# Performance work log

Hardware: AMD Instinct MI355X
Metric: run time of the kernel (lower is better)

## Reference

```python
import jax, jax.numpy as jnp
import numpy as np

T_, N_, DIN, D, HEADS, WW, E_, DPE = 8, 20000, 128, 128, 4, 4, 320000, 8
DH = D // HEADS
NEG = -1e30
EPS_GATE = 1e-6


def setup_inputs() -> dict:
    key = jax.random.key(0)
    ks = jax.random.split(key, 10)
    return {
        "H_tilde": jax.random.normal(ks[0], (T_, N_, DIN), jnp.float32),
        "S": jax.random.uniform(ks[1], (T_, N_), jnp.float32),
        "Wq": jax.random.normal(ks[2], (D, DIN), jnp.float32) * 0.05,
        "Wkh": jax.random.normal(ks[3], (D, DIN), jnp.float32) * 0.05,
        "Wkpe": jax.random.normal(ks[4], (D, DPE), jnp.float32) * 0.05,
        "Wv": jax.random.normal(ks[5], (D, DIN), jnp.float32) * 0.05,
        "pe_table": jax.random.normal(ks[6], (WW + 1, DPE), jnp.float32),
        "rel_bias": jax.random.normal(ks[7], (WW + 1,), jnp.float32),
        "src": jax.random.randint(ks[8], (E_,), 0, N_),
        "dst": jax.random.randint(ks[9], (E_,), 0, N_),
    }


def reference(H_tilde, S, Wq, Wkh, Wkpe, Wv, pe_table, rel_bias, src, dst):
    T, N, _ = H_tilde.shape
    H, dh, W = HEADS, DH, WW
    scale = dh ** -0.5
    dtype = H_tilde.dtype

    # Projections (torch Linear: x @ W.T). W_k over concat([H, pe]) splits additively.
    Q = (H_tilde @ Wq.T).reshape(T, N, H, dh)
    K0 = (H_tilde @ Wkh.T).reshape(T, N, H, dh)
    V = (H_tilde @ Wv.T).reshape(T, N, H, dh)
    pe_k = (pe_table @ Wkpe.T).reshape(W + 1, H, dh)
    gate = jnp.log(jnp.clip(S, 0.0, 1.0) + EPS_GATE)  # (T, N)

    # Pad W zero-steps in front so a length-(W+1) slice at t covers t-W..t.
    pad = lambda x: jnp.concatenate([jnp.zeros((W,) + x.shape[1:], x.dtype), x], axis=0)
    Kp, Vp, gp = pad(K0), pad(V), pad(gate)

    def step(_, tq):
        t, Qt = tq  # Qt: (N, H, dh)
        Kwin = jax.lax.dynamic_slice_in_dim(Kp, t, W + 1, 0)[::-1]  # (W+1,N,H,dh), dt=0..W
        Vwin = jax.lax.dynamic_slice_in_dim(Vp, t, W + 1, 0)[::-1]
        gwin = jax.lax.dynamic_slice_in_dim(gp, t, W + 1, 0)[::-1]  # (W+1, N)
        Qd = Qt[dst]  # (E, H, dh)

        scores = []
        for dt in range(W + 1):
            Ks = Kwin[dt][src] + pe_k[dt][None]  # (E, H, dh)
            s = (jnp.einsum('ehc,ehc->eh', Qd, Ks) * scale
                 + rel_bias[dt] + gwin[dt][src][:, None])
            scores.append(jnp.where(dt <= t, s, NEG))  # mask dt > t (W_eff = min(W, t))
        sc = jnp.stack(scores)  # (W+1, E, H)

        # Segment softmax over incoming edges of each dst node, jointly over dt.
        mx = jax.ops.segment_max(sc.transpose(1, 0, 2), dst, num_segments=N)  # (N,W+1,H)
        mx = mx.max(axis=1)  # (N, H)
        valid = (jnp.arange(W + 1) <= t)[:, None, None]
        ex = jnp.where(valid, jnp.exp(sc - mx[dst][None]), 0.0)  # (W+1, E, H)

        denom = jax.ops.segment_sum(ex.sum(axis=0), dst, num_segments=N)  # (N, H)
        numer = jnp.zeros((N, H, dh), dtype)
        for dt in range(W + 1):
            contrib = ex[dt][:, :, None] * Vwin[dt][src]  # (E, H, dh)
            numer = numer + jax.ops.segment_sum(contrib, dst, num_segments=N)

        msg = numer / jnp.maximum(denom, 1e-12)[:, :, None]  # (N, H, dh)
        return None, msg.reshape(N, H * dh)

    _, M_out = jax.lax.scan(step, None, (jnp.arange(T), Q))
    return M_out  # (T, N, d)
```

## Files before the change

### kernel.cpp

```cpp
#include <hip/hip_runtime.h>

typedef unsigned short u16;
typedef unsigned int u32;
typedef __attribute__((ext_vector_type(8))) __bf16 bf16x8;
typedef __attribute__((ext_vector_type(4))) float f32x4;
typedef __attribute__((ext_vector_type(4))) _Float16 f16x4;
typedef __attribute__((ext_vector_type(2))) unsigned u32x2;

constexpr int TT = 8, NN = 20000, DD = 128, EE = 320000;
constexpr int MAXDEG = 64;
constexpr float SCL = 0.17677669529663687f;
constexpr int VBLK2 = 544;

__device__ __forceinline__ u16 f2bf(float f) {
  return __builtin_bit_cast(u16, (__bf16)f);
}
__device__ __forceinline__ u16 f2h(float f) {
  return __builtin_bit_cast(u16, (_Float16)f);
}
__device__ __forceinline__ float blo(u32 u) { return __uint_as_float(u << 16); }
__device__ __forceinline__ float bhi(u32 u) { return __uint_as_float(u & 0xffff0000u); }

__device__ __forceinline__ bf16x8 cvt8(float4 f0, float4 f1) {
  bf16x8 r;
  r[0] = (__bf16)f0.x; r[1] = (__bf16)f0.y; r[2] = (__bf16)f0.z; r[3] = (__bf16)f0.w;
  r[4] = (__bf16)f1.x; r[5] = (__bf16)f1.y; r[6] = (__bf16)f1.z; r[7] = (__bf16)f1.w;
  return r;
}

__global__ void k_init(const float* __restrict__ pe_table, const float* __restrict__ Wkpe,
                       const float* __restrict__ Wq, const float* __restrict__ Wkh,
                       const float* __restrict__ Wv,
                       float* __restrict__ pek, int* __restrict__ cnt,
                       u16* __restrict__ Wb) {
  int i = blockIdx.x * 256 + threadIdx.x;
  if (i < NN) cnt[i] = 0;
  if (i < 5 * DD) {
    int dt = i >> 7, j = i & 127;
    float s = 0.f;
    for (int p = 0; p < 8; ++p) s += pe_table[dt * 8 + p] * Wkpe[j * 8 + p];
    pek[i] = s;
  }
  if (i < 3 * DD * DD) {
    int y = i / (DD * DD), idx = i % (DD * DD);
    const float* W = (y == 0) ? Wq : (y == 1) ? Wkh : Wv;
    Wb[i] = f2bf(W[idx]);
  }
}

__global__ void k_build(const int* __restrict__ src, const int* __restrict__ dst,
                        int* __restrict__ cnt, int* __restrict__ eslot) {
  int i = blockIdx.x * 256 + threadIdx.x;
  if (i < EE) {
    int d = dst[i];
    int p = atomicAdd(&cnt[d], 1);
    if (p < MAXDEG) eslot[d * MAXDEG + p] = src[i];
  }
}

__global__ __launch_bounds__(256) void k_proj5(
    const float* __restrict__ Hm, const u16* __restrict__ Wb,
    u16* __restrict__ Qb, u16* __restrict__ Kb, u16* __restrict__ Vb) {
  int tid = threadIdx.x;
  int lane = tid & 63, wv = tid >> 6;
  int wr = wv >> 1, wc = wv & 1;
  int l15 = lane & 15, lq = lane >> 4;
  size_t m0 = (size_t)blockIdx.x * 128;

  for (int y = 0; y < 3; ++y) {
    u16* Out = (y == 0) ? Qb : (y == 1) ? Kb : Vb;
    const bool asF16 = (y == 2);
    const u16* Wy = Wb + y * DD * DD;

    f32x4 acc[4][4];
    for (int i = 0; i < 4; ++i)
      for (int j = 0; j < 4; ++j) acc[i][j] = (f32x4){0.f, 0.f, 0.f, 0.f};

    for (int ks = 0; ks < 4; ++ks) {
      int col0 = ks * 32 + lq * 8;
      bf16x8 a[4], b[4];
#pragma unroll
      for (int i = 0; i < 4; ++i) {
        const float* gp = Hm + (m0 + wr * 64 + i * 16 + l15) * DD + col0;
        a[i] = cvt8(*(const float4*)gp, *(const float4*)(gp + 4));
      }
#pragma unroll
      for (int j = 0; j < 4; ++j)
        b[j] = *(const bf16x8*)(Wy + (wc * 64 + j * 16 + l15) * DD + col0);
#pragma unroll
      for (int i = 0; i < 4; ++i)
#pragma unroll
        for (int j = 0; j < 4; ++j)
          acc[i][j] = __builtin_amdgcn_mfma_f32_16x16x32_bf16(a[i], b[j], acc[i][j], 0, 0, 0);
    }

#pragma unroll
    for (int i = 0; i < 4; ++i)
#pragma unroll
      for (int j = 0; j < 4; ++j)
#pragma unroll
        for (int g = 0; g < 4; ++g) {
          size_t row = m0 + wr * 64 + i * 16 + lq * 4 + g;
          int col = wc * 64 + j * 16 + l15;
          Out[row * DD + col] = asF16 ? f2h(acc[i][j][g]) : f2bf(acc[i][j][g]);
        }
  }
}

__global__ __launch_bounds__(256) void k_etab(const u16* __restrict__ Qb,
                                              const float* __restrict__ pek,
                                              const float* __restrict__ relb,
                                              float* __restrict__ Etab) {
  int t = blockIdx.y;
  int n = blockIdx.x * 64 + (threadIdx.x >> 2);
  int h = threadIdx.x & 3;
  if (n >= NN) return;
  const u16* qp = Qb + ((size_t)t * NN + n) * DD + h * 32;
  float q[32];
#pragma unroll
  for (int u = 0; u < 4; ++u) {
    uint4 qv = *(const uint4*)(qp + u * 8);
    q[u*8+0]=blo(qv.x); q[u*8+1]=bhi(qv.x); q[u*8+2]=blo(qv.y); q[u*8+3]=bhi(qv.y);
    q[u*8+4]=blo(qv.z); q[u*8+5]=bhi(qv.z); q[u*8+6]=blo(qv.w); q[u*8+7]=bhi(qv.w);
  }
#pragma unroll
  for (int d = 0; d < 5; ++d) {
    float s = 0.f;
#pragma unroll
    for (int c = 0; c < 32; ++c) s += q[c] * pek[d * DD + h * 32 + c];
    Etab[((size_t)(t * 5 + d) * NN + n) * 4 + h] = __expf(s * SCL + relb[d]);
  }
}

__global__ __launch_bounds__(256, 8) void k_agg8(
    const u16* __restrict__ Qb, const u16* __restrict__ Kb, const u16* __restrict__ Vb,
    const float* __restrict__ Sarr, const float* __restrict__ Etab,
    const int* __restrict__ cnt, const int* __restrict__ eslot,
    float* __restrict__ outp) {
  __shared__ int srcS[MAXDEG];
  __shared__ float eS[40][4];
  __shared__ u16 VldsS[4][VBLK2];
  int tid = threadIdx.x;
  const int h = tid >> 6, lane = tid & 63;
  const int n = blockIdx.x;

  int deg = min(cnt[n], MAXDEG);
  if (tid < MAXDEG) srcS[tid] = (tid < deg) ? eslot[n * MAXDEG + tid] : 0;
  if (tid < 160) {
    int p = tid >> 2, hh = tid & 3;
    eS[p][hh] = Etab[((size_t)p * NN + n) * 4 + hh];
  }
  __syncthreads();

  const int t16 = lane & 15, qo = lane >> 4, qo4 = qo * 4;
  const int h32 = h * 32;

  uint4 qb;
  {
    bool qok = t16 < 8;
    const u16* Qp = Qb + ((size_t)(t16 & 7) * NN + n) * DD + h32 + qo * 8;
    qb = qok ? *(const uint4*)(Qp) : make_uint4(0u, 0u, 0u, 0u);
  }

  f32x4 num0 = (f32x4){0.f, 0.f, 0.f, 0.f};
  f32x4 num1 = (f32x4){0.f, 0.f, 0.f, 0.f};
  float dd = 0.f;

  if (deg > 0) {
    const int degm1 = deg - 1;
    const int nch = (deg + 15) >> 4;
    const int cmax = nch << 4;
    const int nj = nch * 8;

    const int vkey = lane >> 2, vcb = lane & 3;
    u16* vbuf = &VldsS[h][0];
    unsigned trbase = (unsigned)(uintptr_t)vbuf + lane * 8;
    unsigned woff = (unsigned)((vcb >> 1) * VBLK2 + (vkey >> 2) * 128 +
                               (vkey & 3) * 32 + (vcb & 1) * 16);

    auto loadK = [&](int tp, int c16) -> uint4 {
      return *(const uint4*)(Kb + (size_t)tp * (NN * DD)
                             + (size_t)srcS[min(c16 + t16, degm1)] * DD + h32 + qo * 8);
    };
    auto loadV = [&](int tp, int c16) -> uint4 {
      return *(const uint4*)(Vb + (size_t)tp * (NN * DD)
                             + (size_t)srcS[min(c16 + vkey, degm1)] * DD + h32 + vcb * 8);
    };
    auto loadSg = [&](int tp, int c16) -> float {
      float s = Sarr[(size_t)tp * NN + srcS[min(c16 + t16, degm1)]];
      return fminf(fmaxf(s, 0.f), 1.f) + 1e-6f;
    };
    auto writeV = [&](uint4 f) { *(uint4*)((char*)vbuf + woff) = f; };
    auto compute = [&](uint4 ka, float sg, int tp, int c16) {
      int dt = t16 - tp;
      bool tval = (dt >= 0) && (dt <= 4) && (t16 < 8);
      float Ef = tval ? eS[t16 * 5 + dt][h] : 0.f;

      f32x4 z = (f32x4){0.f, 0.f, 0.f, 0.f};
      f32x4 sc = __builtin_amdgcn_mfma_f32_16x16x32_bf16(
          __builtin_bit_cast(bf16x8, ka), __builtin_bit_cast(bf16x8, qb), z, 0, 0, 0);

      f16x4 wf;
      float w0, w1, w2, w3;
      {
        float g0 = __shfl(sg, qo4 + 0), g1 = __shfl(sg, qo4 + 1);
        float g2 = __shfl(sg, qo4 + 2), g3 = __shfl(sg, qo4 + 3);
        g0 = ((c16 + qo4 + 0) < deg) ? g0 : 0.f;
        g1 = ((c16 + qo4 + 1) < deg) ? g1 : 0.f;
        g2 = ((c16 + qo4 + 2) < deg) ? g2 : 0.f;
        g3 = ((c16 + qo4 + 3) < deg) ? g3 : 0.f;
        w0 = __expf(sc[0] * SCL) * Ef * g0;
        w1 = __expf(sc[1] * SCL) * Ef * g1;
        w2 = __expf(sc[2] * SCL) * Ef * g2;
        w3 = __expf(sc[3] * SCL) * Ef * g3;
      }
      dd += w0 + w1 + w2 + w3;
      wf[0] = (_Float16)w0; wf[1] = (_Float16)w1;
      wf[2] = (_Float16)w2; wf[3] = (_Float16)w3;

      __builtin_amdgcn_sched_barrier(0);
      u32x2 vr0, vr1;
      asm volatile("ds_read_b64_tr_b16 %0, %1" : "=v"(vr0) : "v"(trbase));
      asm volatile("ds_read_b64_tr_b16 %0, %1 offset:544" : "=v"(vr1) : "v"(trbase));
      asm volatile("s_waitcnt lgkmcnt(0)");
      __builtin_amdgcn_sched_barrier(0);
      num0 = __builtin_amdgcn_mfma_f32_16x16x16f16(
          wf, __builtin_bit_cast(f16x4, vr0), num0, 0, 0, 0);
      num1 = __builtin_amdgcn_mfma_f32_16x16x16f16(
          wf, __builtin_bit_cast(f16x4, vr1), num1, 0, 0, 0);
    };

    uint4 kA = loadK(0, 0);
    float sgA = loadSg(0, 0);
    writeV(loadV(0, 0));
    int tpj = 0, cj = 0;
    int tpn = 0, cn = 16;
    if (cn >= cmax) { cn = 0; tpn = 1; }

    for (int j = 0; j < nj; ++j) {
      bool more = (j + 1) < nj;
      uint4 kB = make_uint4(0u, 0u, 0u, 0u), vB = make_uint4(0u, 0u, 0u, 0u);
      float sgB = 0.f;
      if (more) {
        kB = loadK(tpn, cn);
        vB = loadV(tpn, cn);
        sgB = loadSg(tpn, cn);
      }
      compute(kA, sgA, tpj, cj);
      __builtin_amdgcn_sched_barrier(0);
      if (more) writeV(vB);
      kA = kB;
      sgA = sgB;
      tpj = tpn; cj = cn;
      cn += 16;
      if (cn >= cmax) { cn = 0; ++tpn; }
    }
  }

  float Dh = dd;
  Dh += __shfl_xor(Dh, 16);
  Dh += __shfl_xor(Dh, 32);
#pragma unroll
  for (int r = 0; r < 4; ++r) {
    int t = qo4 + r;
    float Dt = __shfl(Dh, t);
    if (t < 8) {
      float inv = 1.f / fmaxf(Dt, 1e-12f);
      float* op = outp + ((size_t)t * NN + n) * DD + h32;
      op[t16] = num0[r] * inv;
      op[16 + t16] = num1[r] * inv;
    }
  }
}

extern "C" void kernel_launch(void* const* d_in, const int* in_sizes, int n_in,
                              void* d_out, int out_size, void* d_ws, size_t ws_size,
                              hipStream_t stream) {
  const float* Hm = (const float*)d_in[0];
  const float* S = (const float*)d_in[1];
  const float* Wq = (const float*)d_in[2];
  const float* Wkh = (const float*)d_in[3];
  const float* Wkpe = (const float*)d_in[4];
  const float* Wv = (const float*)d_in[5];
  const float* pe_table = (const float*)d_in[6];
  const float* relb = (const float*)d_in[7];
  const int* src = (const int*)d_in[8];
  const int* dst = (const int*)d_in[9];
  float* out = (float*)d_out;

  auto aup = [](size_t x) { return (x + 255) & ~(size_t)255; };
  char* base = (char*)d_ws;
  size_t off = 0;
  u16* Qb = (u16*)(base + off); off = aup(off + (size_t)TT * NN * DD * 2);
  u16* Kb = (u16*)(base + off); off = aup(off + (size_t)TT * NN * DD * 2);
  u16* Vb = (u16*)(base + off); off = aup(off + (size_t)TT * NN * DD * 2);
  float* pek = (float*)(base + off); off = aup(off + (size_t)5 * DD * 4);
  float* Etab = (float*)(base + off); off = aup(off + (size_t)TT * 5 * NN * 4 * 4);
  int* cnt = (int*)(base + off); off = aup(off + (size_t)NN * 4);
  int* eslot = (int*)(base + off); off = aup(off + (size_t)NN * MAXDEG * 4);
  u16* Wb = (u16*)(base + off); off = aup(off + (size_t)3 * DD * DD * 2);
  (void)ws_size; (void)in_sizes; (void)n_in; (void)out_size;

  k_init<<<(3 * DD * DD + 255) / 256, 256, 0, stream>>>(pe_table, Wkpe, Wq, Wkh, Wv,
                                                        pek, cnt, Wb);
  k_build<<<(EE + 255) / 256, 256, 0, stream>>>(src, dst, cnt, eslot);
  k_proj5<<<1250, 256, 0, stream>>>(Hm, Wb, Qb, Kb, Vb);
  k_etab<<<dim3((NN + 63) / 64, TT), 256, 0, stream>>>(Qb, pek, relb, Etab);
  k_agg8<<<NN, 256, 0, stream>>>(Qb, Kb, Vb, S, Etab, cnt, eslot, out);
}
```

Measured before the change: 365.2 us.

## Fuse edge-bias table into aggregation and reorder loop edge-chunk-outer, time-inner

Removes the separate k_etab kernel and its Etab buffer. The aggregation kernel now computes the per-node Q·pe_k plus rel_bias logits itself, using lane shuffles, and stores them in LDS. The clamped gate S is precomputed once in k_init into SgT. The main loop changes to edge-chunk outer and time-step inner, so each neighbour index and its offsets are fetched once and reused across all 8 timesteps, and the bias is folded into the exp argument. This saves one kernel launch and a global table round-trip, and moves the gate values to LDS per step. In exchange each block does a little more prologue work and adds LDS writes and reads per step.

```diff
diff --git a/kernel.cpp b/kernel.cpp
--- a/kernel.cpp
+++ b/kernel.cpp
@@ -30,9 +30,9 @@
 
 __global__ void k_init(const float* __restrict__ pe_table, const float* __restrict__ Wkpe,
                        const float* __restrict__ Wq, const float* __restrict__ Wkh,
-                       const float* __restrict__ Wv,
+                       const float* __restrict__ Wv, const float* __restrict__ S,
                        float* __restrict__ pek, int* __restrict__ cnt,
-                       u16* __restrict__ Wb) {
+                       u16* __restrict__ Wb, float* __restrict__ SgT) {
   int i = blockIdx.x * 256 + threadIdx.x;
   if (i < NN) cnt[i] = 0;
   if (i < 5 * DD) {
@@ -45,6 +45,9 @@
     int y = i / (DD * DD), idx = i % (DD * DD);
     const float* W = (y == 0) ? Wq : (y == 1) ? Wkh : Wv;
     Wb[i] = f2bf(W[idx]);
+  }
+  if (i < TT * NN) {
+    SgT[i] = fminf(fmaxf(S[i], 0.f), 1.f) + 1e-6f;
   }
 }
 
@@ -107,38 +110,15 @@
   }
 }
 
-__global__ __launch_bounds__(256) void k_etab(const u16* __restrict__ Qb,
-                                              const float* __restrict__ pek,
-                                              const float* __restrict__ relb,
-                                              float* __restrict__ Etab) {
-  int t = blockIdx.y;
-  int n = blockIdx.x * 64 + (threadIdx.x >> 2);
-  int h = threadIdx.x & 3;
-  if (n >= NN) return;
-  const u16* qp = Qb + ((size_t)t * NN + n) * DD + h * 32;
-  float q[32];
-#pragma unroll
-  for (int u = 0; u < 4; ++u) {
-    uint4 qv = *(const uint4*)(qp + u * 8);
-    q[u*8+0]=blo(qv.x); q[u*8+1]=bhi(qv.x); q[u*8+2]=blo(qv.y); q[u*8+3]=bhi(qv.y);
-    q[u*8+4]=blo(qv.z); q[u*8+5]=bhi(qv.z); q[u*8+6]=blo(qv.w); q[u*8+7]=bhi(qv.w);
-  }
-#pragma unroll
-  for (int d = 0; d < 5; ++d) {
-    float s = 0.f;
-#pragma unroll
-    for (int c = 0; c < 32; ++c) s += q[c] * pek[d * DD + h * 32 + c];
-    Etab[((size_t)(t * 5 + d) * NN + n) * 4 + h] = __expf(s * SCL + relb[d]);
-  }
-}
-
-__global__ __launch_bounds__(256, 8) void k_agg8(
+__global__ __launch_bounds__(256, 8) void k_agg9(
     const u16* __restrict__ Qb, const u16* __restrict__ Kb, const u16* __restrict__ Vb,
-    const float* __restrict__ Sarr, const float* __restrict__ Etab,
+    const float* __restrict__ SgT, const float* __restrict__ pek,
+    const float* __restrict__ relb,
     const int* __restrict__ cnt, const int* __restrict__ eslot,
     float* __restrict__ outp) {
   __shared__ int srcS[MAXDEG];
-  __shared__ float eS[40][4];
+  __shared__ float eL[4][40];
+  __shared__ float sgS[4][16];
   __shared__ u16 VldsS[4][VBLK2];
   int tid = threadIdx.x;
   const int h = tid >> 6, lane = tid & 63;
@@ -146,14 +126,10 @@
 
   int deg = min(cnt[n], MAXDEG);
   if (tid < MAXDEG) srcS[tid] = (tid < deg) ? eslot[n * MAXDEG + tid] : 0;
-  if (tid < 160) {
-    int p = tid >> 2, hh = tid & 3;
-    eS[p][hh] = Etab[((size_t)p * NN + n) * 4 + hh];
-  }
-  __syncthreads();
 
   const int t16 = lane & 15, qo = lane >> 4, qo4 = qo * 4;
   const int h32 = h * 32;
+  const int e6 = t16 * 6;
 
   uint4 qb;
   {
@@ -162,98 +138,98 @@
     qb = qok ? *(const uint4*)(Qp) : make_uint4(0u, 0u, 0u, 0u);
   }
 
+  {
+    float qf0 = blo(qb.x), qf1 = bhi(qb.x), qf2 = blo(qb.y), qf3 = bhi(qb.y);
+    float qf4 = blo(qb.z), qf5 = bhi(qb.z), qf6 = blo(qb.w), qf7 = bhi(qb.w);
+#pragma unroll
+    for (int d = 0; d < 5; ++d) {
+      const float* pp = pek + d * DD + h32 + qo * 8;
+      float4 p0 = *(const float4*)pp;
+      float4 p1 = *(const float4*)(pp + 4);
+      float s = qf0 * p0.x + qf1 * p0.y + qf2 * p0.z + qf3 * p0.w
+              + qf4 * p1.x + qf5 * p1.y + qf6 * p1.z + qf7 * p1.w;
+      s += __shfl_xor(s, 16);
+      s += __shfl_xor(s, 32);
+      if (qo == 0 && t16 < 8) eL[h][t16 * 5 + d] = s * SCL + relb[d];
+    }
+  }
+  __syncthreads();
+
   f32x4 num0 = (f32x4){0.f, 0.f, 0.f, 0.f};
   f32x4 num1 = (f32x4){0.f, 0.f, 0.f, 0.f};
   float dd = 0.f;
 
   if (deg > 0) {
     const int degm1 = deg - 1;
-    const int nch = (deg + 15) >> 4;
-    const int cmax = nch << 4;
-    const int nj = nch * 8;
-
-    const int vkey = lane >> 2, vcb = lane & 3;
     u16* vbuf = &VldsS[h][0];
     unsigned trbase = (unsigned)(uintptr_t)vbuf + lane * 8;
+    const int vkey = lane >> 2, vcb = lane & 3;
     unsigned woff = (unsigned)((vcb >> 1) * VBLK2 + (vkey >> 2) * 128 +
                                (vkey & 3) * 32 + (vcb & 1) * 16);
 
-    auto loadK = [&](int tp, int c16) -> uint4 {
-      return *(const uint4*)(Kb + (size_t)tp * (NN * DD)
-                             + (size_t)srcS[min(c16 + t16, degm1)] * DD + h32 + qo * 8);
-    };
-    auto loadV = [&](int tp, int c16) -> uint4 {
-      return *(const uint4*)(Vb + (size_t)tp * (NN * DD)
-                             + (size_t)srcS[min(c16 + vkey, degm1)] * DD + h32 + vcb * 8);
-    };
-    auto loadSg = [&](int tp, int c16) -> float {
-      float s = Sarr[(size_t)tp * NN + srcS[min(c16 + t16, degm1)]];
-      return fminf(fmaxf(s, 0.f), 1.f) + 1e-6f;
-    };
-    auto writeV = [&](uint4 f) { *(uint4*)((char*)vbuf + woff) = f; };
-    auto compute = [&](uint4 ka, float sg, int tp, int c16) {
-      int dt = t16 - tp;
-      bool tval = (dt >= 0) && (dt <= 4) && (t16 < 8);
-      float Ef = tval ? eS[t16 * 5 + dt][h] : 0.f;
-
-      f32x4 z = (f32x4){0.f, 0.f, 0.f, 0.f};
-      f32x4 sc = __builtin_amdgcn_mfma_f32_16x16x32_bf16(
-          __builtin_bit_cast(bf16x8, ka), __builtin_bit_cast(bf16x8, qb), z, 0, 0, 0);
-
-      f16x4 wf;
-      float w0, w1, w2, w3;
-      {
-        float g0 = __shfl(sg, qo4 + 0), g1 = __shfl(sg, qo4 + 1);
-        float g2 = __shfl(sg, qo4 + 2), g3 = __shfl(sg, qo4 + 3);
-        g0 = ((c16 + qo4 + 0) < deg) ? g0 : 0.f;
-        g1 = ((c16 + qo4 + 1) < deg) ? g1 : 0.f;
-        g2 = ((c16 + qo4 + 2) < deg) ? g2 : 0.f;
-        g3 = ((c16 + qo4 + 3) < deg) ? g3 : 0.f;
-        w0 = __expf(sc[0] * SCL) * Ef * g0;
-        w1 = __expf(sc[1] * SCL) * Ef * g1;
-        w2 = __expf(sc[2] * SCL) * Ef * g2;
-        w3 = __expf(sc[3] * SCL) * Ef * g3;
+    for (int c16 = 0; c16 < deg; c16 += 16) {
+      int nK = srcS[min(c16 + t16, degm1)];
+      int nV = srcS[min(c16 + vkey, degm1)];
+      bool kmask = (c16 + t16) < deg;
+      size_t offK = (size_t)nK * DD + h32 + qo * 8;
+      size_t offV = (size_t)nV * DD + h32 + vcb * 8;
+
+      uint4 kA = *(const uint4*)(Kb + offK);
+      uint4 vA = *(const uint4*)(Vb + offV);
+      float sA;
+      { float sv = SgT[nK]; sA = kmask ? sv : 0.f; }
+      *(uint4*)((char*)vbuf + woff) = vA;
+
+#pragma unroll
+      for (int tp = 0; tp < 8; ++tp) {
+        uint4 kB = make_uint4(0u, 0u, 0u, 0u), vB = make_uint4(0u, 0u, 0u, 0u);
+        float sB = 0.f;
+        if (tp < 7) {
+          kB = *(const uint4*)(Kb + (size_t)(tp + 1) * (NN * DD) + offK);
+          vB = *(const uint4*)(Vb + (size_t)(tp + 1) * (NN * DD) + offV);
+          float sv = SgT[(tp + 1) * NN + nK];
+          sB = kmask ? sv : 0.f;
+        }
+
+        if (qo == 0) sgS[h][t16] = sA;
+        f32x4 z = (f32x4){0.f, 0.f, 0.f, 0.f};
+        f32x4 sc = __builtin_amdgcn_mfma_f32_16x16x32_bf16(
+            __builtin_bit_cast(bf16x8, kA), __builtin_bit_cast(bf16x8, qb), z, 0, 0, 0);
+        f32x4 sg4 = *(const f32x4*)&sgS[h][qo4];
+
+        int dt = t16 - tp;
+        bool valid = ((unsigned)dt <= 4u) && (t16 < 8);
+        int idxE = valid ? (e6 - tp) : 0;
+        float Lf = eL[h][idxE];
+        Lf = valid ? Lf : -1e30f;
+
+        float w0 = __expf(sc[0] * SCL + Lf) * sg4[0];
+        float w1 = __expf(sc[1] * SCL + Lf) * sg4[1];
+        float w2 = __expf(sc[2] * SCL + Lf) * sg4[2];
+        float w3 = __expf(sc[3] * SCL + Lf) * sg4[3];
+        dd += w0 + w1 + w2 + w3;
+        f16x4 wf;
+        wf[0] = (_Float16)w0; wf[1] = (_Float16)w1;
+        wf[2] = (_Float16)w2; wf[3] = (_Float16)w3;
+
+        __builtin_amdgcn_sched_barrier(0);
+        u32x2 vr0, vr1;
+        asm volatile("ds_read_b64_tr_b16 %0, %1" : "=v"(vr0) : "v"(trbase));
+        asm volatile("ds_read_b64_tr_b16 %0, %1 offset:544" : "=v"(vr1) : "v"(trbase));
+        asm volatile("s_waitcnt lgkmcnt(0)");
+        __builtin_amdgcn_sched_barrier(0);
+        num0 = __builtin_amdgcn_mfma_f32_16x16x16f16(
+            wf, __builtin_bit_cast(f16x4, vr0), num0, 0, 0, 0);
+        num1 = __builtin_amdgcn_mfma_f32_16x16x16f16(
+            wf, __builtin_bit_cast(f16x4, vr1), num1, 0, 0, 0);
+
+        __builtin_amdgcn_sched_barrier(0);
+        if (tp < 7) {
+          *(uint4*)((char*)vbuf + woff) = vB;
+          kA = kB;
+          sA = sB;
+        }
       }
-      dd += w0 + w1 + w2 + w3;
-      wf[0] = (_Float16)w0; wf[1] = (_Float16)w1;
-      wf[2] = (_Float16)w2; wf[3] = (_Float16)w3;
-
-      __builtin_amdgcn_sched_barrier(0);
-      u32x2 vr0, vr1;
-      asm volatile("ds_read_b64_tr_b16 %0, %1" : "=v"(vr0) : "v"(trbase));
-      asm volatile("ds_read_b64_tr_b16 %0, %1 offset:544" : "=v"(vr1) : "v"(trbase));
-      asm volatile("s_waitcnt lgkmcnt(0)");
-      __builtin_amdgcn_sched_barrier(0);
-      num0 = __builtin_amdgcn_mfma_f32_16x16x16f16(
-          wf, __builtin_bit_cast(f16x4, vr0), num0, 0, 0, 0);
-      num1 = __builtin_amdgcn_mfma_f32_16x16x16f16(
-          wf, __builtin_bit_cast(f16x4, vr1), num1, 0, 0, 0);
-    };
-
-    uint4 kA = loadK(0, 0);
-    float sgA = loadSg(0, 0);
-    writeV(loadV(0, 0));
-    int tpj = 0, cj = 0;
-    int tpn = 0, cn = 16;
-    if (cn >= cmax) { cn = 0; tpn = 1; }
-
-    for (int j = 0; j < nj; ++j) {
-      bool more = (j + 1) < nj;
-      uint4 kB = make_uint4(0u, 0u, 0u, 0u), vB = make_uint4(0u, 0u, 0u, 0u);
-      float sgB = 0.f;
-      if (more) {
-        kB = loadK(tpn, cn);
-        vB = loadV(tpn, cn);
-        sgB = loadSg(tpn, cn);
-      }
-      compute(kA, sgA, tpj, cj);
-      __builtin_amdgcn_sched_barrier(0);
-      if (more) writeV(vB);
-      kA = kB;
-      sgA = sgB;
-      tpj = tpn; cj = cn;
-      cn += 16;
-      if (cn >= cmax) { cn = 0; ++tpn; }
     }
   }
 
@@ -295,16 +271,15 @@
   u16* Kb = (u16*)(base + off); off = aup(off + (size_t)TT * NN * DD * 2);
   u16* Vb = (u16*)(base + off); off = aup(off + (size_t)TT * NN * DD * 2);
   float* pek = (float*)(base + off); off = aup(off + (size_t)5 * DD * 4);
-  float* Etab = (float*)(base + off); off = aup(off + (size_t)TT * 5 * NN * 4 * 4);
+  float* SgT = (float*)(base + off); off = aup(off + (size_t)TT * NN * 4);
   int* cnt = (int*)(base + off); off = aup(off + (size_t)NN * 4);
   int* eslot = (int*)(base + off); off = aup(off + (size_t)NN * MAXDEG * 4);
   u16* Wb = (u16*)(base + off); off = aup(off + (size_t)3 * DD * DD * 2);
   (void)ws_size; (void)in_sizes; (void)n_in; (void)out_size;
 
-  k_init<<<(3 * DD * DD + 255) / 256, 256, 0, stream>>>(pe_table, Wkpe, Wq, Wkh, Wv,
-                                                        pek, cnt, Wb);
+  k_init<<<(TT * NN + 255) / 256, 256, 0, stream>>>(pe_table, Wkpe, Wq, Wkh, Wv, S,
+                                                    pek, cnt, Wb, SgT);
   k_build<<<(EE + 255) / 256, 256, 0, stream>>>(src, dst, cnt, eslot);
   k_proj5<<<1250, 256, 0, stream>>>(Hm, Wb, Qb, Kb, Vb);
-  k_etab<<<dim3((NN + 63) / 64, TT), 256, 0, stream>>>(Qb, pek, relb, Etab);
-  k_agg8<<<NN, 256, 0, stream>>>(Qb, Kb, Vb, S, Etab, cnt, eslot, out);
-}
+  k_agg9<<<NN, 256, 0, stream>>>(Qb, Kb, Vb, SgT, pek, relb, cnt, eslot, out);
+}
```

Result: slower. 598.6 us (+63.9%).

## Fuse Etab computation into aggregation, precompute gate, hoist H loads in projection

Applied to the files above, without the earlier changes.

Drops the separate k_etab kernel. Each aggregation block now computes its own q·pe_k exponentials from the Q fragment it already holds, reducing across lanes with shuffles. The clamped gate S+eps is precomputed once in k_init, so the gather loop no longer clamps per edge. k_proj6 loads and converts the H tile to bf16 once and reuses it across the Q/K/V passes instead of reloading it three times, at the cost of more live registers.

```diff
diff --git a/kernel.cpp b/kernel.cpp
--- a/kernel.cpp
+++ b/kernel.cpp
@@ -30,9 +30,9 @@
 
 __global__ void k_init(const float* __restrict__ pe_table, const float* __restrict__ Wkpe,
                        const float* __restrict__ Wq, const float* __restrict__ Wkh,
-                       const float* __restrict__ Wv,
+                       const float* __restrict__ Wv, const float* __restrict__ S,
                        float* __restrict__ pek, int* __restrict__ cnt,
-                       u16* __restrict__ Wb) {
+                       u16* __restrict__ Wb, float* __restrict__ SgT) {
   int i = blockIdx.x * 256 + threadIdx.x;
   if (i < NN) cnt[i] = 0;
   if (i < 5 * DD) {
@@ -46,6 +46,9 @@
     const float* W = (y == 0) ? Wq : (y == 1) ? Wkh : Wv;
     Wb[i] = f2bf(W[idx]);
   }
+  if (i < TT * NN) {
+    SgT[i] = fminf(fmaxf(S[i], 0.f), 1.f) + 1e-6f;
+  }
 }
 
 __global__ void k_build(const int* __restrict__ src, const int* __restrict__ dst,
@@ -58,7 +61,7 @@
   }
 }
 
-__global__ __launch_bounds__(256) void k_proj5(
+__global__ __launch_bounds__(256) void k_proj6(
     const float* __restrict__ Hm, const u16* __restrict__ Wb,
     u16* __restrict__ Qb, u16* __restrict__ Kb, u16* __restrict__ Vb) {
   int tid = threadIdx.x;
@@ -67,6 +70,17 @@
   int l15 = lane & 15, lq = lane >> 4;
   size_t m0 = (size_t)blockIdx.x * 128;
 
+  bf16x8 a[4][4];
+#pragma unroll
+  for (int ks = 0; ks < 4; ++ks) {
+    int col0 = ks * 32 + lq * 8;
+#pragma unroll
+    for (int i = 0; i < 4; ++i) {
+      const float* gp = Hm + (m0 + wr * 64 + i * 16 + l15) * DD + col0;
+      a[ks][i] = cvt8(*(const float4*)gp, *(const float4*)(gp + 4));
+    }
+  }
+
   for (int y = 0; y < 3; ++y) {
     u16* Out = (y == 0) ? Qb : (y == 1) ? Kb : Vb;
     const bool asF16 = (y == 2);
@@ -78,12 +92,7 @@
 
     for (int ks = 0; ks < 4; ++ks) {
       int col0 = ks * 32 + lq * 8;
-      bf16x8 a[4], b[4];
-#pragma unroll
-      for (int i = 0; i < 4; ++i) {
-        const float* gp = Hm + (m0 + wr * 64 + i * 16 + l15) * DD + col0;
-        a[i] = cvt8(*(const float4*)gp, *(const float4*)(gp + 4));
-      }
+      bf16x8 b[4];
 #pragma unroll
       for (int j = 0; j < 4; ++j)
         b[j] = *(const bf16x8*)(Wy + (wc * 64 + j * 16 + l15) * DD + col0);
@@ -91,7 +100,7 @@
       for (int i = 0; i < 4; ++i)
 #pragma unroll
         for (int j = 0; j < 4; ++j)
-          acc[i][j] = __builtin_amdgcn_mfma_f32_16x16x32_bf16(a[i], b[j], acc[i][j], 0, 0, 0);
+          acc[i][j] = __builtin_amdgcn_mfma_f32_16x16x32_bf16(a[ks][i], b[j], acc[i][j], 0, 0, 0);
     }
 
 #pragma unroll
@@ -107,38 +116,14 @@
   }
 }
 
-__global__ __launch_bounds__(256) void k_etab(const u16* __restrict__ Qb,
-                                              const float* __restrict__ pek,
-                                              const float* __restrict__ relb,
-                                              float* __restrict__ Etab) {
-  int t = blockIdx.y;
-  int n = blockIdx.x * 64 + (threadIdx.x >> 2);
-  int h = threadIdx.x & 3;
-  if (n >= NN) return;
-  const u16* qp = Qb + ((size_t)t * NN + n) * DD + h * 32;
-  float q[32];
-#pragma unroll
-  for (int u = 0; u < 4; ++u) {
-    uint4 qv = *(const uint4*)(qp + u * 8);
-    q[u*8+0]=blo(qv.x); q[u*8+1]=bhi(qv.x); q[u*8+2]=blo(qv.y); q[u*8+3]=bhi(qv.y);
-    q[u*8+4]=blo(qv.z); q[u*8+5]=bhi(qv.z); q[u*8+6]=blo(qv.w); q[u*8+7]=bhi(qv.w);
-  }
-#pragma unroll
-  for (int d = 0; d < 5; ++d) {
-    float s = 0.f;
-#pragma unroll
-    for (int c = 0; c < 32; ++c) s += q[c] * pek[d * DD + h * 32 + c];
-    Etab[((size_t)(t * 5 + d) * NN + n) * 4 + h] = __expf(s * SCL + relb[d]);
-  }
-}
-
-__global__ __launch_bounds__(256, 8) void k_agg8(
+__global__ __launch_bounds__(256, 8) void k_agg10(
     const u16* __restrict__ Qb, const u16* __restrict__ Kb, const u16* __restrict__ Vb,
-    const float* __restrict__ Sarr, const float* __restrict__ Etab,
+    const float* __restrict__ SgT, const float* __restrict__ pek,
+    const float* __restrict__ relb,
     const int* __restrict__ cnt, const int* __restrict__ eslot,
     float* __restrict__ outp) {
   __shared__ int srcS[MAXDEG];
-  __shared__ float eS[40][4];
+  __shared__ float eS2[4][40];
   __shared__ u16 VldsS[4][VBLK2];
   int tid = threadIdx.x;
   const int h = tid >> 6, lane = tid & 63;
@@ -146,11 +131,6 @@
 
   int deg = min(cnt[n], MAXDEG);
   if (tid < MAXDEG) srcS[tid] = (tid < deg) ? eslot[n * MAXDEG + tid] : 0;
-  if (tid < 160) {
-    int p = tid >> 2, hh = tid & 3;
-    eS[p][hh] = Etab[((size_t)p * NN + n) * 4 + hh];
-  }
-  __syncthreads();
 
   const int t16 = lane & 15, qo = lane >> 4, qo4 = qo * 4;
   const int h32 = h * 32;
@@ -161,6 +141,23 @@
     const u16* Qp = Qb + ((size_t)(t16 & 7) * NN + n) * DD + h32 + qo * 8;
     qb = qok ? *(const uint4*)(Qp) : make_uint4(0u, 0u, 0u, 0u);
   }
+
+  {
+    float qf0 = blo(qb.x), qf1 = bhi(qb.x), qf2 = blo(qb.y), qf3 = bhi(qb.y);
+    float qf4 = blo(qb.z), qf5 = bhi(qb.z), qf6 = blo(qb.w), qf7 = bhi(qb.w);
+#pragma unroll
+    for (int d = 0; d < 5; ++d) {
+      const float* pp = pek + d * DD + h32 + qo * 8;
+      float4 p0 = *(const float4*)pp;
+      float4 p1 = *(const float4*)(pp + 4);
+      float s = qf0 * p0.x + qf1 * p0.y + qf2 * p0.z + qf3 * p0.w
+              + qf4 * p1.x + qf5 * p1.y + qf6 * p1.z + qf7 * p1.w;
+      s += __shfl_xor(s, 16);
+      s += __shfl_xor(s, 32);
+      if (qo == 0 && t16 < 8) eS2[h][t16 * 5 + d] = __expf(s * SCL + relb[d]);
+    }
+  }
+  __syncthreads();
 
   f32x4 num0 = (f32x4){0.f, 0.f, 0.f, 0.f};
   f32x4 num1 = (f32x4){0.f, 0.f, 0.f, 0.f};
@@ -187,14 +184,13 @@
                              + (size_t)srcS[min(c16 + vkey, degm1)] * DD + h32 + vcb * 8);
     };
     auto loadSg = [&](int tp, int c16) -> float {
-      float s = Sarr[(size_t)tp * NN + srcS[min(c16 + t16, degm1)]];
-      return fminf(fmaxf(s, 0.f), 1.f) + 1e-6f;
+      return SgT[(size_t)tp * NN + srcS[min(c16 + t16, degm1)]];
     };
     auto writeV = [&](uint4 f) { *(uint4*)((char*)vbuf + woff) = f; };
     auto compute = [&](uint4 ka, float sg, int tp, int c16) {
       int dt = t16 - tp;
       bool tval = (dt >= 0) && (dt <= 4) && (t16 < 8);
-      float Ef = tval ? eS[t16 * 5 + dt][h] : 0.f;
+      float Ef = tval ? eS2[h][t16 * 5 + dt] : 0.f;
 
       f32x4 z = (f32x4){0.f, 0.f, 0.f, 0.f};
       f32x4 sc = __builtin_amdgcn_mfma_f32_16x16x32_bf16(
@@ -295,16 +291,15 @@
   u16* Kb = (u16*)(base + off); off = aup(off + (size_t)TT * NN * DD * 2);
   u16* Vb = (u16*)(base + off); off = aup(off + (size_t)TT * NN * DD * 2);
   float* pek = (float*)(base + off); off = aup(off + (size_t)5 * DD * 4);
-  float* Etab = (float*)(base + off); off = aup(off + (size_t)TT * 5 * NN * 4 * 4);
+  float* SgT = (float*)(base + off); off = aup(off + (size_t)TT * NN * 4);
   int* cnt = (int*)(base + off); off = aup(off + (size_t)NN * 4);
   int* eslot = (int*)(base + off); off = aup(off + (size_t)NN * MAXDEG * 4);
   u16* Wb = (u16*)(base + off); off = aup(off + (size_t)3 * DD * DD * 2);
   (void)ws_size; (void)in_sizes; (void)n_in; (void)out_size;
 
-  k_init<<<(3 * DD * DD + 255) / 256, 256, 0, stream>>>(pe_table, Wkpe, Wq, Wkh, Wv,
-                                                        pek, cnt, Wb);
+  k_init<<<(TT * NN + 255) / 256, 256, 0, stream>>>(pe_table, Wkpe, Wq, Wkh, Wv, S,
+                                                    pek, cnt, Wb, SgT);
   k_build<<<(EE + 255) / 256, 256, 0, stream>>>(src, dst, cnt, eslot);
-  k_proj5<<<1250, 256, 0, stream>>>(Hm, Wb, Qb, Kb, Vb);
-  k_etab<<<dim3((NN + 63) / 64, TT), 256, 0, stream>>>(Qb, pek, relb, Etab);
-  k_agg8<<<NN, 256, 0, stream>>>(Qb, Kb, Vb, S, Etab, cnt, eslot, out);
-}
+  k_proj6<<<1250, 256, 0, stream>>>(Hm, Wb, Qb, Kb, Vb);
+  k_agg10<<<NN, 256, 0, stream>>>(Qb, Kb, Vb, SgT, pek, relb, cnt, eslot, out);
+}
```

Result: faster. 309.4 us (-15.3%).
